# Kernel optimization log

Measured on AMD Instinct MI355X. Metric: run time of the kernel, lower is better.

The kernel has to match this reference:

```python
import jax, jax.numpy as jnp
import numpy as np

NH, KD, HD = 8, 32, 32          # n_heads, qk dim, value dim per head
D = NH * HD                     # 256 channels (v.reshape requires d == nh*hd)
SCALE = 0.17677669529663687     # kd ** -0.5


def setup_inputs() -> dict:
    key = jax.random.key(0)
    k1, k2 = jax.random.split(key)
    x = jax.random.normal(k1, (2, D, 64, 64), dtype=jnp.float32)
    # dp[1]: bias-free 1x1 conv D -> NH*(4*KD+HD) = 1280, fan-in scaled
    w_proj = jax.random.normal(k2, (NH * (4 * KD + HD), D), dtype=jnp.float32) * np.float32(1.0 / np.sqrt(D))
    return {"x": x, "w_proj": w_proj}


def reference(x, w_proj):
    b, d, h, w = x.shape
    # dp[0] = Identity; dp[1] = 1x1 conv as a channel matmul
    p = jnp.einsum('bchw,oc->bohw', x, w_proj).reshape(b, NH, 4 * KD + HD, h, w)
    rq = p[:, :, 0 * KD:1 * KD]
    rk = p[:, :, 1 * KD:2 * KD]
    cq = p[:, :, 2 * KD:3 * KD]
    ck = p[:, :, 3 * KD:4 * KD]
    v = p[:, :, 4 * KD:]                      # (b, NH, HD, h, w)
    # row attention over h (independently per column w), softmax over i (dim 2)
    r = jax.nn.softmax(jnp.einsum('bHdiw,bHdjw->bHijw', rq, rk) * SCALE, axis=2)
    # column attention over w (independently per row h), softmax over i (dim 2)
    c = jax.nn.softmax(jnp.einsum('bHdhi,bHdhj->bHihj', cq, ck) * SCALE, axis=2)
    # trilinear combine: out[b,H,d,h,w] = sum_{i,j} r[b,H,i,h,w] * v[b,H,d,i,j] * c[b,H,j,h,w]
    # contract v with c first, then with r (intermediate m is (b,NH,HD,h,h,w))
    m = jnp.einsum('bHdij,bHjhw->bHdihw', v, c)
    out = jnp.einsum('bHihw,bHdihw->bHdhw', r, m).reshape(b, d, h, w)
    # residual: dp[2] = Identity, dp[3] = Identity
    return out + v.reshape(b, d, h, w)
```

## Files before the change

### kernel.cpp

```cpp
#include <hip/hip_runtime.h>
#include <stdint.h>


#define SCALE 0.17677669529663687f
typedef unsigned short ushort_t;
typedef __attribute__((ext_vector_type(8))) short bf16x8;
typedef __attribute__((ext_vector_type(4))) float f32x4;

__device__ __forceinline__ unsigned short f2bf(float f) {
  unsigned int b = __float_as_uint(f);
  b += 0x7fffu + ((b >> 16) & 1u);
  return (unsigned short)(b >> 16);
}
__device__ __forceinline__ float bflo(unsigned int u) { return __uint_as_float(u << 16); }
__device__ __forceinline__ float bfhi(unsigned int u) { return __uint_as_float(u & 0xffff0000u); }
__device__ __forceinline__ unsigned int pk2(float a, float b) {
  return (unsigned int)f2bf(a) | ((unsigned int)f2bf(b) << 16);
}
__device__ __forceinline__ f32x4 mfma16(bf16x8 a, bf16x8 b, f32x4 c) {
  return __builtin_amdgcn_mfma_f32_16x16x32_bf16(a, b, c, 0, 0, 0);
}
__device__ __forceinline__ void gld16(const void* g, void* l) {
  __builtin_amdgcn_global_load_lds(
      (const __attribute__((address_space(1))) unsigned int*)g,
      (__attribute__((address_space(3))) unsigned int*)l, 16, 0, 0);
}

__global__ __launch_bounds__(256) void prep(const float* __restrict__ x,
                                            const float* __restrict__ w,
                                            ushort_t* __restrict__ xtf,
                                            ushort_t* __restrict__ wf) {
  const int bid = blockIdx.x;
  const int t = threadIdx.x;
  if (bid < 512) {
    __shared__ float tile[128][33];
    const int b = bid >> 8, rem = bid & 255;
    const int kc = rem >> 5;
    const int n0 = (rem & 31) * 128;
    const float* xb = x + (size_t)b * 256 * 4096;
#pragma unroll
    for (int rep = 0; rep < 4; rep++) {
      int idx = rep * 256 + t;
      int kk = idx >> 5, nn4 = (idx & 31) * 4;
      float4 f = *(const float4*)&xb[(size_t)(kc * 32 + kk) * 4096 + n0 + nn4];
      tile[nn4 + 0][kk] = f.x; tile[nn4 + 1][kk] = f.y;
      tile[nn4 + 2][kk] = f.z; tile[nn4 + 3][kk] = f.w;
    }
    __syncthreads();
    ushort_t* xo = xtf + (size_t)b * 1048576;
#pragma unroll
    for (int rep = 0; rep < 2; rep++) {
      int idx = rep * 256 + t;
      int n = idx >> 2, k8 = (idx & 3) * 8;
      uint4 o;
      o.x = pk2(tile[n][k8 + 0], tile[n][k8 + 1]);
      o.y = pk2(tile[n][k8 + 2], tile[n][k8 + 3]);
      o.z = pk2(tile[n][k8 + 4], tile[n][k8 + 5]);
      o.w = pk2(tile[n][k8 + 6], tile[n][k8 + 7]);
      int nt = (n0 + n) >> 4;
      int lane = ((n0 + n) & 15) + ((k8 >> 3) << 4);
      *(uint4*)&xo[(size_t)((nt * 8 + kc) * 64 + lane) * 8] = o;
    }
  } else {
    const int mt = bid - 512;
    const int wv = t >> 6, l = t & 63;
#pragma unroll
    for (int s = 0; s < 2; s++) {
      int kc = wv + s * 4;
      const float* src = &w[(size_t)(mt * 16 + (l & 15)) * 256 + kc * 32 + (l >> 4) * 8];
      float4 f0 = *(const float4*)&src[0];
      float4 f1 = *(const float4*)&src[4];
      uint4 o;
      o.x = pk2(f0.x, f0.y); o.y = pk2(f0.z, f0.w);
      o.z = pk2(f1.x, f1.y); o.w = pk2(f1.z, f1.w);
      *(uint4*)&wf[(size_t)((mt * 8 + kc) * 64 + l) * 8] = o;
    }
  }
}

__global__ __launch_bounds__(256, 4) void proj_mfma_v3(const ushort_t* __restrict__ wf,
                                                       const ushort_t* __restrict__ xtf,
                                                       ushort_t* __restrict__ Qr,
                                                       ushort_t* __restrict__ Kr,
                                                       ushort_t* __restrict__ Qc,
                                                       ushort_t* __restrict__ Kc,
                                                       float* __restrict__ P_v) {
  const int b = blockIdx.z, by = blockIdx.y, bx = blockIdx.x;
  const int m0 = by * 128, n0 = bx * 128;
  const int t = threadIdx.x, wv = t >> 6, l = t & 63;
  const int row = l & 15, quad = l >> 4;
  const int wm = wv >> 1, wn = wv & 1;
  const ushort_t* xb = xtf + (size_t)b * 1048576;

  f32x4 acc[4][4];
#pragma unroll
  for (int i = 0; i < 4; i++)
#pragma unroll
    for (int j = 0; j < 4; j++) acc[i][j] = (f32x4){0.f, 0.f, 0.f, 0.f};

  const size_t abase = (size_t)(by * 8 + wm * 4) * 4096 + l * 8;
  const size_t bbase = (size_t)(bx * 8 + wn * 4) * 4096 + l * 8;

  for (int kc = 0; kc < 8; kc++) {
    bf16x8 af[4], bfr[4];
#pragma unroll
    for (int mf = 0; mf < 4; mf++)
      af[mf] = *(const bf16x8*)&wf[abase + mf * 4096 + kc * 512];
#pragma unroll
    for (int nf = 0; nf < 4; nf++)
      bfr[nf] = *(const bf16x8*)&xb[bbase + nf * 4096 + kc * 512];
#pragma unroll
    for (int mf = 0; mf < 4; mf++)
#pragma unroll
      for (int nf = 0; nf < 4; nf++)
        acc[mf][nf] = mfma16(af[mf], bfr[nf], acc[mf][nf]);
  }

#pragma unroll
  for (int mf = 0; mf < 4; mf++) {
    int mb = m0 + wm * 64 + mf * 16 + quad * 4;
    int H = mb / 160;
    int rem = mb - H * 160;
    int sec = rem >> 5;
    int d0 = rem & 31;
    int bh = b * 8 + H;
    if (sec < 4) {
      ushort_t* base = (sec == 0) ? Qr : (sec == 1) ? Kr : (sec == 2) ? Qc : Kc;
      base += (size_t)bh * 131072;
#pragma unroll
      for (int nf = 0; nf < 4; nf++) {
        int n = n0 + wn * 64 + nf * 16 + row;
        int orow = (sec < 2) ? ((n & 63) * 64 + (n >> 6)) : n;
        uint2 o;
        o.x = pk2(acc[mf][nf][0], acc[mf][nf][1]);
        o.y = pk2(acc[mf][nf][2], acc[mf][nf][3]);
        *(uint2*)&base[(size_t)orow * 32 + d0] = o;
      }
    } else {
      float* pvb = P_v + ((size_t)bh * 32 + d0) * 4096;
#pragma unroll
      for (int nf = 0; nf < 4; nf++) {
        int n = n0 + wn * 64 + nf * 16 + row;
#pragma unroll
        for (int r = 0; r < 4; r++)
          pvb[(size_t)r * 4096 + n] = acc[mf][nf][r];
      }
    }
  }
}

__global__ __launch_bounds__(256) void mid(const ushort_t* __restrict__ Qr,
                                           const ushort_t* __restrict__ Kr,
                                           const ushort_t* __restrict__ Qc,
                                           const ushort_t* __restrict__ Kc,
                                           ushort_t* __restrict__ Rs,
                                           ushort_t* __restrict__ Cs,
                                           const float* __restrict__ P_v,
                                           ushort_t* __restrict__ vf) {
  __shared__ float tile[8][64][33];
  const int bid = blockIdx.x;
  const int t = threadIdx.x, wv = t >> 6, l = t & 63;
  if (bid < 512) {
    const int mode = bid >> 8;
    const int idx = bid & 255;
    const int bh = idx >> 4, gq = idx & 15;
    const int col = l & 15, quad = l >> 4;
    const int g = gq * 4 + wv;
    const ushort_t* Qb = (mode ? Qc : Qr) + (size_t)bh * 131072 + (size_t)g * 2048;
    const ushort_t* Kb = (mode ? Kc : Kr) + (size_t)bh * 131072 + (size_t)g * 2048;

    bf16x8 aq[4], bk[4];
#pragma unroll
    for (int f = 0; f < 4; f++) {
      aq[f] = *(const bf16x8*)&Qb[(size_t)(f * 16 + col) * 32 + quad * 8];
      bk[f] = *(const bf16x8*)&Kb[(size_t)(f * 16 + col) * 32 + quad * 8];
    }
    f32x4 s[4][4];
#pragma unroll
    for (int i0 = 0; i0 < 4; i0++)
#pragma unroll
      for (int j0 = 0; j0 < 4; j0++)
        s[i0][j0] = mfma16(aq[i0], bk[j0], (f32x4){0.f, 0.f, 0.f, 0.f});

    ushort_t* ob = (mode ? Cs : Rs) + (size_t)bh * 262144;
#pragma unroll
    for (int j0 = 0; j0 < 4; j0++) {
      float sv[16];
#pragma unroll
      for (int i0 = 0; i0 < 4; i0++)
#pragma unroll
        for (int r = 0; r < 4; r++) sv[i0 * 4 + r] = s[i0][j0][r] * SCALE;
      float mx = sv[0];
#pragma unroll
      for (int q = 1; q < 16; q++) mx = fmaxf(mx, sv[q]);
      mx = fmaxf(mx, __shfl_xor(mx, 16));
      mx = fmaxf(mx, __shfl_xor(mx, 32));
      float e[16], sum = 0.f;
#pragma unroll
      for (int q = 0; q < 16; q++) { e[q] = __expf(sv[q] - mx); sum += e[q]; }
      sum += __shfl_xor(sum, 16);
      sum += __shfl_xor(sum, 32);
      const float inv = 1.f / sum;
      const int j = j0 * 16 + col;
#pragma unroll
      for (int i0 = 0; i0 < 4; i0++) {
        uint2 o;
        o.x = pk2(e[i0 * 4 + 0] * inv, e[i0 * 4 + 1] * inv);
        o.y = pk2(e[i0 * 4 + 2] * inv, e[i0 * 4 + 3] * inv);
        size_t addr = mode ? ((size_t)(g * 64 + j) * 64 + i0 * 16 + quad * 4)
                           : ((size_t)(j * 64 + g) * 64 + i0 * 16 + quad * 4);
        *(uint2*)&ob[addr] = o;
      }
    }
  } else {
    const int vid = bid - 512;
    const int jc = vid & 7, bh = vid >> 3;
    const int j0 = jc * 8;
    const float* pvb = P_v + (size_t)bh * 131072;
#pragma unroll
    for (int rep = 0; rep < 8; rep++) {
      int idx = rep * 256 + t;
      int d = idx >> 6, i = idx & 63;
      float4 f0 = *(const float4*)&pvb[(size_t)d * 4096 + i * 64 + j0];
      float4 f1 = *(const float4*)&pvb[(size_t)d * 4096 + i * 64 + j0 + 4];
      tile[0][i][d] = f0.x; tile[1][i][d] = f0.y;
      tile[2][i][d] = f0.z; tile[3][i][d] = f0.w;
      tile[4][i][d] = f1.x; tile[5][i][d] = f1.y;
      tile[6][i][d] = f1.z; tile[7][i][d] = f1.w;
    }
    __syncthreads();
    ushort_t* vo = vf + (size_t)bh * 131072;
    const int fid = t >> 6;
    const int d = (fid & 1) * 16 + (l & 15);
    const int i0 = (fid >> 1) * 32 + (l >> 4) * 8;
#pragma unroll
    for (int rep = 0; rep < 8; rep++) {
      int jl = rep;
      uint4 o;
      o.x = pk2(tile[jl][i0 + 0][d], tile[jl][i0 + 1][d]);
      o.y = pk2(tile[jl][i0 + 2][d], tile[jl][i0 + 3][d]);
      o.z = pk2(tile[jl][i0 + 4][d], tile[jl][i0 + 5][d]);
      o.w = pk2(tile[jl][i0 + 6][d], tile[jl][i0 + 7][d]);
      *(uint4*)&vo[(size_t)(((j0 + jl) * 4 + fid) * 64 + l) * 8] = o;
    }
  }
}

__global__ __launch_bounds__(256, 2) void attn_apply_v4(const float* __restrict__ P_v,
                                                        const ushort_t* __restrict__ rs,
                                                        const ushort_t* __restrict__ cs,
                                                        const ushort_t* __restrict__ vf,
                                                        float* __restrict__ out,
                                                        float* __restrict__ pp1) {
  __shared__ ushort_t buf[2][16384];
  const int bid = blockIdx.x;
  const int jc = bid & 1, pg = (bid >> 1) & 15, bh = bid >> 5;
  const int b = bh >> 3, H = bh & 7;
  const int t = threadIdx.x, wv = t >> 6, l = t & 63;
  const int row = l & 15, quad = l >> 4;
  const int h = pg * 4 + wv;
  const ushort_t* rsl = rs + (size_t)bh * 262144 + (size_t)h * 4096;
  const ushort_t* csl = cs + (size_t)bh * 262144 + (size_t)h * 4096;
  const ushort_t* vchunk = vf + (size_t)bh * 131072 + (size_t)jc * 65536;

  bf16x8 rf[2][4];
#pragma unroll
  for (int nf = 0; nf < 4; nf++)
#pragma unroll
    for (int kc = 0; kc < 2; kc++)
      rf[kc][nf] = *(const bf16x8*)&rsl[(size_t)(nf * 16 + row) * 64 + kc * 32 + quad * 8];

  f32x4 acc[2][4];
#pragma unroll
  for (int i = 0; i < 2; i++)
#pragma unroll
    for (int j = 0; j < 4; j++) acc[i][j] = (f32x4){0.f, 0.f, 0.f, 0.f};

#pragma unroll
  for (int jj = 0; jj < 8; jj++)
    gld16(&vchunk[(size_t)jj * 2048 + wv * 512 + l * 8], &buf[0][jj * 2048 + wv * 512]);
  __syncthreads();

  for (int ph = 0; ph < 4; ph++) {
    const ushort_t* bcur = buf[ph & 1];
    if (ph < 3) {
#pragma unroll
      for (int jj = 0; jj < 8; jj++)
        gld16(&vchunk[(size_t)((ph + 1) * 8 + jj) * 2048 + wv * 512 + l * 8],
              &buf[(ph + 1) & 1][jj * 2048 + wv * 512]);
    }
    float cv[8][4];
#pragma unroll
    for (int nf = 0; nf < 4; nf++) {
      uint4 u = *(const uint4*)&csl[(size_t)(nf * 16 + row) * 64 + jc * 32 + ph * 8];
      cv[0][nf] = bflo(u.x); cv[1][nf] = bfhi(u.x);
      cv[2][nf] = bflo(u.y); cv[3][nf] = bfhi(u.y);
      cv[4][nf] = bflo(u.z); cv[5][nf] = bfhi(u.z);
      cv[6][nf] = bflo(u.w); cv[7][nf] = bfhi(u.w);
    }
#pragma unroll
    for (int jj = 0; jj < 8; jj++) {
      bf16x8 af0[2], af1[2];
#pragma unroll
      for (int mf = 0; mf < 2; mf++) {
        af0[mf] = *(const bf16x8*)&bcur[jj * 2048 + (0 + mf) * 512 + l * 8];
        af1[mf] = *(const bf16x8*)&bcur[jj * 2048 + (2 + mf) * 512 + l * 8];
      }
#pragma unroll
      for (int mf = 0; mf < 2; mf++)
#pragma unroll
        for (int nf = 0; nf < 4; nf++) {
          f32x4 tt = (f32x4){0.f, 0.f, 0.f, 0.f};
          tt = mfma16(af0[mf], rf[0][nf], tt);
          tt = mfma16(af1[mf], rf[1][nf], tt);
          acc[mf][nf] += tt * cv[jj][nf];
        }
    }
    __syncthreads();
  }

  if (jc == 0) {
    const float* pv = P_v + (size_t)bh * 131072 + h * 64;
    float* ob = out + ((size_t)b * 256 + H * 32) * 4096 + h * 64;
#pragma unroll
    for (int mf = 0; mf < 2; mf++)
#pragma unroll
      for (int nf = 0; nf < 4; nf++)
#pragma unroll
        for (int reg = 0; reg < 4; reg++) {
          int d = mf * 16 + quad * 4 + reg;
          int wc = nf * 16 + row;
          ob[(size_t)d * 4096 + wc] = acc[mf][nf][reg] + pv[(size_t)d * 4096 + wc];
        }
  } else {
    float* ob = pp1 + (size_t)bh * 131072 + h * 64;
#pragma unroll
    for (int mf = 0; mf < 2; mf++)
#pragma unroll
      for (int nf = 0; nf < 4; nf++)
#pragma unroll
        for (int reg = 0; reg < 4; reg++) {
          int d = mf * 16 + quad * 4 + reg;
          int wc = nf * 16 + row;
          ob[(size_t)d * 4096 + wc] = acc[mf][nf][reg];
        }
  }
}

__global__ __launch_bounds__(256) void sum_out(float* __restrict__ out,
                                               const float* __restrict__ pp1) {
  const int idx = (blockIdx.x * 256 + threadIdx.x) * 4;
  float4 a = *(const float4*)&out[idx];
  float4 b = *(const float4*)&pp1[idx];
  a.x += b.x; a.y += b.y; a.z += b.z; a.w += b.w;
  *(float4*)&out[idx] = a;
}

extern "C" void kernel_launch(void* const* d_in, const int* in_sizes, int n_in,
                              void* d_out, int out_size, void* d_ws, size_t ws_size,
                              hipStream_t stream) {
  const float* x = (const float*)d_in[0];
  const float* w = (const float*)d_in[1];
  float* out = (float*)d_out;
  float* ws = (float*)d_ws;
  float* P_v = ws;
  ushort_t* Rs  = (ushort_t*)(ws + 2097152);
  ushort_t* Cs  = (ushort_t*)(ws + 4194304);
  ushort_t* Vf  = (ushort_t*)(ws + 6291456);
  ushort_t* Qr  = (ushort_t*)(ws + 7340032);
  ushort_t* Kr  = (ushort_t*)(ws + 8388608);
  ushort_t* Qc  = (ushort_t*)(ws + 9437184);
  ushort_t* Kc  = (ushort_t*)(ws + 10485760);
  ushort_t* Wf  = (ushort_t*)(ws + 11534336);
  ushort_t* Xtf = (ushort_t*)(ws + 11698176);
  float* Pp1 = ws + 12746752;

  prep<<<592, 256, 0, stream>>>(x, w, Xtf, Wf);
  proj_mfma_v3<<<dim3(32, 10, 2), 256, 0, stream>>>(Wf, Xtf, Qr, Kr, Qc, Kc, P_v);
  mid<<<640, 256, 0, stream>>>(Qr, Kr, Qc, Kc, Rs, Cs, P_v, Vf);
  attn_apply_v4<<<512, 256, 0, stream>>>(P_v, Rs, Cs, Vf, out, Pp1);
  sum_out<<<2048, 256, 0, stream>>>(out, Pp1);
}
```

Measured before the change: 120.1 us.

## Split attention apply over value-dim halves instead of j-halves, drop reduction kernel

Changes the work split of the apply kernel. Each block pair now covers the two halves of the value dimension d over the full j range, where before it covered the two halves of j. Each block now produces final outputs directly, so the partial-sum buffer and the separate sum_out kernel are gone, removing a launch and a full read-modify-write pass over the output. In exchange each block streams twice as many j steps, with a smaller LDS buffer and fewer MFMAs per step, and recomputes the same MFMAs for the r-side operand.

New measurement: 122.7 us. 2.2% more time.

```diff
diff --git a/kernel.cpp b/kernel.cpp
--- a/kernel.cpp
+++ b/kernel.cpp
@@ -246,22 +246,21 @@
   }
 }
 
-__global__ __launch_bounds__(256, 2) void attn_apply_v4(const float* __restrict__ P_v,
+__global__ __launch_bounds__(256, 2) void attn_apply_v5(const float* __restrict__ P_v,
                                                         const ushort_t* __restrict__ rs,
                                                         const ushort_t* __restrict__ cs,
                                                         const ushort_t* __restrict__ vf,
-                                                        float* __restrict__ out,
-                                                        float* __restrict__ pp1) {
-  __shared__ ushort_t buf[2][16384];
+                                                        float* __restrict__ out) {
+  __shared__ ushort_t buf[2][8192];
   const int bid = blockIdx.x;
-  const int jc = bid & 1, pg = (bid >> 1) & 15, bh = bid >> 5;
+  const int ds = bid & 1, pg = (bid >> 1) & 15, bh = bid >> 5;
   const int b = bh >> 3, H = bh & 7;
   const int t = threadIdx.x, wv = t >> 6, l = t & 63;
   const int row = l & 15, quad = l >> 4;
   const int h = pg * 4 + wv;
   const ushort_t* rsl = rs + (size_t)bh * 262144 + (size_t)h * 4096;
   const ushort_t* csl = cs + (size_t)bh * 262144 + (size_t)h * 4096;
-  const ushort_t* vchunk = vf + (size_t)bh * 131072 + (size_t)jc * 65536;
+  const ushort_t* vb = vf + (size_t)bh * 131072;
 
   bf16x8 rf[2][4];
 #pragma unroll
@@ -270,29 +269,33 @@
     for (int kc = 0; kc < 2; kc++)
       rf[kc][nf] = *(const bf16x8*)&rsl[(size_t)(nf * 16 + row) * 64 + kc * 32 + quad * 8];
 
-  f32x4 acc[2][4];
-#pragma unroll
-  for (int i = 0; i < 2; i++)
-#pragma unroll
-    for (int j = 0; j < 4; j++) acc[i][j] = (f32x4){0.f, 0.f, 0.f, 0.f};
-
-#pragma unroll
-  for (int jj = 0; jj < 8; jj++)
-    gld16(&vchunk[(size_t)jj * 2048 + wv * 512 + l * 8], &buf[0][jj * 2048 + wv * 512]);
+  f32x4 acc[4];
+#pragma unroll
+  for (int nf = 0; nf < 4; nf++) acc[nf] = (f32x4){0.f, 0.f, 0.f, 0.f};
+
+#pragma unroll
+  for (int u = 0; u < 4; u++) {
+    int idx = u * 256 + t;
+    int jj = idx >> 7, kcl = (idx >> 6) & 1, ll = idx & 63;
+    gld16(&vb[(size_t)((jj * 4 + ds + 2 * kcl) * 64 + ll) * 8], &buf[0][idx * 8]);
+  }
   __syncthreads();
 
-  for (int ph = 0; ph < 4; ph++) {
+  for (int ph = 0; ph < 8; ph++) {
     const ushort_t* bcur = buf[ph & 1];
-    if (ph < 3) {
-#pragma unroll
-      for (int jj = 0; jj < 8; jj++)
-        gld16(&vchunk[(size_t)((ph + 1) * 8 + jj) * 2048 + wv * 512 + l * 8],
-              &buf[(ph + 1) & 1][jj * 2048 + wv * 512]);
+    if (ph < 7) {
+#pragma unroll
+      for (int u = 0; u < 4; u++) {
+        int idx = u * 256 + t;
+        int jj = idx >> 7, kcl = (idx >> 6) & 1, ll = idx & 63;
+        gld16(&vb[(size_t)(((ph + 1) * 8 + jj) * 4 + ds + 2 * kcl) * 64 * 8 + ll * 8],
+              &buf[(ph + 1) & 1][idx * 8]);
+      }
     }
     float cv[8][4];
 #pragma unroll
     for (int nf = 0; nf < 4; nf++) {
-      uint4 u = *(const uint4*)&csl[(size_t)(nf * 16 + row) * 64 + jc * 32 + ph * 8];
+      uint4 u = *(const uint4*)&csl[(size_t)(nf * 16 + row) * 64 + ph * 8];
       cv[0][nf] = bflo(u.x); cv[1][nf] = bfhi(u.x);
       cv[2][nf] = bflo(u.y); cv[3][nf] = bfhi(u.y);
       cv[4][nf] = bflo(u.z); cv[5][nf] = bfhi(u.z);
@@ -300,60 +303,29 @@
     }
 #pragma unroll
     for (int jj = 0; jj < 8; jj++) {
-      bf16x8 af0[2], af1[2];
-#pragma unroll
-      for (int mf = 0; mf < 2; mf++) {
-        af0[mf] = *(const bf16x8*)&bcur[jj * 2048 + (0 + mf) * 512 + l * 8];
-        af1[mf] = *(const bf16x8*)&bcur[jj * 2048 + (2 + mf) * 512 + l * 8];
-      }
-#pragma unroll
-      for (int mf = 0; mf < 2; mf++)
-#pragma unroll
-        for (int nf = 0; nf < 4; nf++) {
-          f32x4 tt = (f32x4){0.f, 0.f, 0.f, 0.f};
-          tt = mfma16(af0[mf], rf[0][nf], tt);
-          tt = mfma16(af1[mf], rf[1][nf], tt);
-          acc[mf][nf] += tt * cv[jj][nf];
-        }
+      bf16x8 a0 = *(const bf16x8*)&bcur[((jj * 2 + 0) * 64 + l) * 8];
+      bf16x8 a1 = *(const bf16x8*)&bcur[((jj * 2 + 1) * 64 + l) * 8];
+#pragma unroll
+      for (int nf = 0; nf < 4; nf++) {
+        f32x4 tt = (f32x4){0.f, 0.f, 0.f, 0.f};
+        tt = mfma16(a0, rf[0][nf], tt);
+        tt = mfma16(a1, rf[1][nf], tt);
+        acc[nf] += tt * cv[jj][nf];
+      }
     }
     __syncthreads();
   }
 
-  if (jc == 0) {
-    const float* pv = P_v + (size_t)bh * 131072 + h * 64;
-    float* ob = out + ((size_t)b * 256 + H * 32) * 4096 + h * 64;
-#pragma unroll
-    for (int mf = 0; mf < 2; mf++)
-#pragma unroll
-      for (int nf = 0; nf < 4; nf++)
-#pragma unroll
-        for (int reg = 0; reg < 4; reg++) {
-          int d = mf * 16 + quad * 4 + reg;
-          int wc = nf * 16 + row;
-          ob[(size_t)d * 4096 + wc] = acc[mf][nf][reg] + pv[(size_t)d * 4096 + wc];
-        }
-  } else {
-    float* ob = pp1 + (size_t)bh * 131072 + h * 64;
-#pragma unroll
-    for (int mf = 0; mf < 2; mf++)
-#pragma unroll
-      for (int nf = 0; nf < 4; nf++)
-#pragma unroll
-        for (int reg = 0; reg < 4; reg++) {
-          int d = mf * 16 + quad * 4 + reg;
-          int wc = nf * 16 + row;
-          ob[(size_t)d * 4096 + wc] = acc[mf][nf][reg];
-        }
-  }
-}
-
-__global__ __launch_bounds__(256) void sum_out(float* __restrict__ out,
-                                               const float* __restrict__ pp1) {
-  const int idx = (blockIdx.x * 256 + threadIdx.x) * 4;
-  float4 a = *(const float4*)&out[idx];
-  float4 b = *(const float4*)&pp1[idx];
-  a.x += b.x; a.y += b.y; a.z += b.z; a.w += b.w;
-  *(float4*)&out[idx] = a;
+  const float* pv = P_v + (size_t)bh * 131072 + h * 64;
+  float* ob = out + ((size_t)b * 256 + H * 32) * 4096 + h * 64;
+#pragma unroll
+  for (int nf = 0; nf < 4; nf++)
+#pragma unroll
+    for (int reg = 0; reg < 4; reg++) {
+      int d = ds * 16 + quad * 4 + reg;
+      int wc = nf * 16 + row;
+      ob[(size_t)d * 4096 + wc] = acc[nf][reg] + pv[(size_t)d * 4096 + wc];
+    }
 }
 
 extern "C" void kernel_launch(void* const* d_in, const int* in_sizes, int n_in,
@@ -373,11 +345,9 @@
   ushort_t* Kc  = (ushort_t*)(ws + 10485760);
   ushort_t* Wf  = (ushort_t*)(ws + 11534336);
   ushort_t* Xtf = (ushort_t*)(ws + 11698176);
-  float* Pp1 = ws + 12746752;
 
   prep<<<592, 256, 0, stream>>>(x, w, Xtf, Wf);
   proj_mfma_v3<<<dim3(32, 10, 2), 256, 0, stream>>>(Wf, Xtf, Qr, Kr, Qc, Kc, P_v);
   mid<<<640, 256, 0, stream>>>(Qr, Kr, Qc, Kc, Rs, Cs, P_v, Vf);
-  attn_apply_v4<<<512, 256, 0, stream>>>(P_v, Rs, Cs, Vf, out, Pp1);
-  sum_out<<<2048, 256, 0, stream>>>(out, Pp1);
-}
+  attn_apply_v5<<<512, 256, 0, stream>>>(P_v, Rs, Cs, Vf, out);
+}
```
